# Kernel optimization log

Hardware: AMD Instinct MI355X
Metric: run time of the kernel (lower is better)

The kernel has to match this reference:

```python
import jax, jax.numpy as jnp
import numpy as np

B, D_IN, D_BN, K = 4096, 4096, 32768, 64

def setup_inputs() -> dict:
    key = jax.random.key(0)
    k1, k2, k3 = jax.random.split(key, 3)
    x = jax.random.normal(k1, (B, D_IN), dtype=jnp.float32)
    # encoder weight [bottleneck, input], kaiming-ish scale
    W_enc = jax.random.normal(k2, (D_BN, D_IN), dtype=jnp.float32) / np.sqrt(D_IN)
    b_enc = jax.random.normal(k3, (D_BN,), dtype=jnp.float32) * 0.01
    b_dec = jnp.zeros((D_IN,), dtype=jnp.float32)
    return {"x": x, "W_enc": W_enc, "b_enc": b_enc, "b_dec": b_dec, "k": K}

def reference(x, W_enc, b_enc, b_dec, k):
    # encode: z1 = x @ W_enc.T + b_enc  -> [B, bottleneck]
    a1 = jnp.einsum('bi,ni->bn', x, W_enc) + b_enc
    # top-k winner-take-all mask along latent dim (eval path: current_k = k)
    k_count = min(max(1, int(k)), a1.shape[1])
    _, topk_idx = jax.lax.top_k(a1, k_count)              # [B, k]
    rows = jnp.arange(a1.shape[0])[:, None]
    mask = jnp.zeros_like(a1).at[rows, topk_idx].set(1.0)
    a1 = a1 * mask
    # tied-weight decode: z2 = a1 @ W_enc + b_dec  -> [B, input]
    z2 = jnp.einsum('bn,ni->bi', a1, W_enc) + b_dec
    return z2
```

## Files before the change

kernel.cpp:

```cpp
#include <hip/hip_runtime.h>

#define M_DIM 4096
#define K_DIM 4096
#define N_DIM 32768
#define TOPK  64
#define NCAND 96
#define NT    (K_DIM / 64)

typedef __attribute__((ext_vector_type(8))) _Float16 half8;
typedef __attribute__((ext_vector_type(4))) _Float16 half4;
typedef __attribute__((ext_vector_type(4))) float    f32x4;

#define GLDS(gp, lp) __builtin_amdgcn_global_load_lds( \
    (const __attribute__((address_space(1))) void*)(gp), \
    (__attribute__((address_space(3))) void*)(lp), 16, 0, 0)

#define BARX()  asm volatile("s_barrier" ::: "memory")
#define LGKM0() asm volatile("s_waitcnt lgkmcnt(0)" ::: "memory")
#define VMC6()  asm volatile("s_waitcnt vmcnt(6)" ::: "memory")
#define VMC0()  asm volatile("s_waitcnt vmcnt(0)" ::: "memory")

__launch_bounds__(256)
__global__ void cast_kernel(const float4* __restrict__ src, half4* __restrict__ dst, int n4) {
  int i = blockIdx.x * blockDim.x + threadIdx.x;
  int stride = gridDim.x * blockDim.x;
  for (; i < n4; i += stride) {
    float4 x = src[i];
    half4 h;
    h[0] = (_Float16)x.x; h[1] = (_Float16)x.y; h[2] = (_Float16)x.z; h[3] = (_Float16)x.w;
    dst[i] = h;
  }
}

__launch_bounds__(512, 2)
__global__ void gemm_enc(const _Float16* __restrict__ xh, const _Float16* __restrict__ wh,
                         const float* __restrict__ b_enc, float* __restrict__ a1)
{
  __shared__ alignas(16) _Float16 lds[2 * 4 * 8192];

  const int tid  = threadIdx.x;
  const int lane = tid & 63;
  const int wave = tid >> 6;
  const int wm = wave >> 2;
  const int wn = wave & 3;

  const int bid  = blockIdx.x;
  const int xcd  = bid & 7;
  const int bi   = bid >> 3;
  const int ncol = xcd * 16 + (bi >> 4);
  const int mrow = bi & 15;
  const int m0 = mrow << 8;
  const int n0 = ncol << 8;

  const int srow   = tid >> 3;
  const int schunk = (tid & 7) ^ (srow & 7);
  const _Float16* pA = xh + (size_t)(m0 + srow) * K_DIM + schunk * 8;
  const _Float16* pB = wh + (size_t)(n0 + srow) * K_DIM + schunk * 8;
  const int sdst = tid * 8;

  const int l15 = lane & 15, l7 = lane & 7, kq = lane >> 4;
  const int c0  = kq ^ l7;
  const int ck0 = c0 * 8, ck1 = (c0 ^ 4) * 8;
  const int arow = l15 * 64;
  const int brow = (wn & 1) * 4096 + l15 * 64;

  f32x4 acc[8][4];
  const f32x4 zero = {0.f, 0.f, 0.f, 0.f};
#pragma unroll
  for (int im = 0; im < 8; ++im)
#pragma unroll
    for (int jn = 0; jn < 4; ++jn) acc[im][jn] = zero;

#define STAGE(c, t) do { \
    const _Float16* sp_ = (((c) >= 2) ? pA : pB) + (size_t)((c) & 1) * 128 * K_DIM + (t) * 64; \
    _Float16* dp_ = &lds[(((((t) & 1) << 2) | (c)) << 13) + sdst]; \
    GLDS(sp_, dp_); \
    GLDS(sp_ + 64 * K_DIM, dp_ + 4096); \
  } while (0)

  half8 a_[4][2], b_[4][2];

#define LDA(mh, ab) do { \
    _Pragma("unroll") for (int mt = 0; mt < 4; ++mt) { \
      a_[mt][0] = *(const half8*)&lds[(ab) + (mh) * 4096 + mt * 1024 + arow + ck0]; \
      a_[mt][1] = *(const half8*)&lds[(ab) + (mh) * 4096 + mt * 1024 + arow + ck1]; \
    } } while (0)

#define LDB(bb) do { \
    _Pragma("unroll") for (int nt = 0; nt < 4; ++nt) { \
      b_[nt][0] = *(const half8*)&lds[(bb) + nt * 1024 + brow + ck0]; \
      b_[nt][1] = *(const half8*)&lds[(bb) + nt * 1024 + brow + ck1]; \
    } } while (0)

#define QUAD(mh, nh) do { \
    _Pragma("unroll") for (int mt = 0; mt < 4; ++mt) \
    _Pragma("unroll") for (int nt = 0; nt < 2; ++nt) { \
      acc[(mh)*4+mt][(nh)*2+nt] = __builtin_amdgcn_mfma_f32_16x16x32_f16( \
          a_[mt][0], b_[(nh)*2+nt][0], acc[(mh)*4+mt][(nh)*2+nt], 0, 0, 0); \
      acc[(mh)*4+mt][(nh)*2+nt] = __builtin_amdgcn_mfma_f32_16x16x32_f16( \
          a_[mt][1], b_[(nh)*2+nt][1], acc[(mh)*4+mt][(nh)*2+nt], 0, 0, 0); \
    } } while (0)

  STAGE(0, 0); STAGE(1, 0); STAGE(2, 0); STAGE(3, 0);
  STAGE(0, 1); STAGE(1, 1); STAGE(2, 1);
  VMC6();
  BARX();

  for (int T = 0; T < NT; ++T) {
    const int ab = (((T & 1) << 2) + 2 + wm) << 13;
    const int bb = (((T & 1) << 2) + (wn >> 1)) << 13;
    LDA(0, ab);
    LDB(bb);
    if (T + 1 < NT) STAGE(3, T + 1);
    BARX(); LGKM0();
    __builtin_amdgcn_s_setprio(1); QUAD(0, 0); __builtin_amdgcn_s_setprio(0);
    BARX();
    if (T + 2 < NT) STAGE(0, T + 2);
    BARX();
    __builtin_amdgcn_s_setprio(1); QUAD(0, 1); __builtin_amdgcn_s_setprio(0);
    BARX();
    LDA(1, ab);
    if (T + 2 < NT) STAGE(1, T + 2);
    BARX(); LGKM0();
    __builtin_amdgcn_s_setprio(1); QUAD(1, 0); __builtin_amdgcn_s_setprio(0);
    BARX();
    if (T + 2 < NT) STAGE(2, T + 2);
    BARX();
    __builtin_amdgcn_s_setprio(1); QUAD(1, 1); __builtin_amdgcn_s_setprio(0);
    if (T < NT - 2) { VMC6(); } else { VMC0(); }
    BARX();
  }

  const int col = lane & 15;
  const int r4  = (lane >> 4) << 2;
#pragma unroll
  for (int nt = 0; nt < 4; ++nt) {
    const int gc = n0 + wn * 64 + nt * 16 + col;
    const float bias = b_enc[gc];
#pragma unroll
    for (int mt = 0; mt < 8; ++mt) {
#pragma unroll
      for (int r = 0; r < 4; ++r) {
        const int gr = m0 + wm * 128 + mt * 16 + r4 + r;
        a1[(size_t)gr * N_DIM + gc] = acc[mt][nt][r] + bias;
      }
    }
  }
#undef STAGE
#undef LDA
#undef LDB
#undef QUAD
}

#define TK_THREADS 512
#define TK_PER 64
__launch_bounds__(512)
__global__ void topk_kernel(const float* __restrict__ a1, int* __restrict__ cand)
{
  const int row = blockIdx.x;
  const float* pr = a1 + (size_t)row * N_DIM;
  const int tid = threadIdx.x;

  unsigned u[TK_PER];
#pragma unroll
  for (int i = 0; i < TK_PER; ++i) {
    union { float f; unsigned b; } c;
    c.f = pr[i * TK_THREADS + tid];
    u[i] = (c.b & 0x80000000u) ? ~c.b : (c.b | 0x80000000u);
  }

  __shared__ int red[8];
  unsigned prefix = 0;
  int needed = NCAND;
  for (int bit = 31; bit >= 0; --bit) {
    unsigned want = (prefix >> bit) | 1u;
    int cnt = 0;
#pragma unroll
    for (int i = 0; i < TK_PER; ++i) cnt += ((u[i] >> bit) == want) ? 1 : 0;
    for (int off = 32; off > 0; off >>= 1) cnt += __shfl_down(cnt, off);
    if ((tid & 63) == 0) red[tid >> 6] = cnt;
    __syncthreads();
    int total = red[0] + red[1] + red[2] + red[3] + red[4] + red[5] + red[6] + red[7];
    __syncthreads();
    if (total >= needed) prefix |= (1u << bit);
    else needed -= total;
  }
  __shared__ int c_gt, c_tie;
  if (tid == 0) { c_gt = 0; c_tie = 0; }
  __syncthreads();
#pragma unroll
  for (int i = 0; i < TK_PER; ++i) {
    if (u[i] > prefix) {
      int p = atomicAdd(&c_gt, 1);
      cand[row * NCAND + p] = i * TK_THREADS + tid;
    }
  }
  __syncthreads();
  int base = c_gt;
#pragma unroll
  for (int i = 0; i < TK_PER; ++i) {
    if (u[i] == prefix) {
      int t = atomicAdd(&c_tie, 1);
      if (t < needed) cand[row * NCAND + base + t] = i * TK_THREADS + tid;
    }
  }
}

__launch_bounds__(256)
__global__ void refine_kernel(const float* __restrict__ x, const float* __restrict__ W,
                              const float* __restrict__ b_enc, const int* __restrict__ cand,
                              int* __restrict__ tk_idx, float* __restrict__ tk_val)
{
  const int row = blockIdx.x;
  const int tid = threadIdx.x, lane = tid & 63, wave = tid >> 6;
  __shared__ float svals[NCAND];
  __shared__ int   sidx[NCAND];
  __shared__ int   spos;

  const float* xr = x + (size_t)row * K_DIM;
  float4 xv[16];
#pragma unroll
  for (int c = 0; c < 16; ++c) xv[c] = *(const float4*)(xr + c * 256 + lane * 4);

  for (int j = wave; j < NCAND; j += 4) {
    int cj = cand[row * NCAND + j];
    const float* wr = W + (size_t)cj * K_DIM;
    float acc = 0.f;
#pragma unroll
    for (int c = 0; c < 16; ++c) {
      float4 wv = *(const float4*)(wr + c * 256 + lane * 4);
      acc += xv[c].x * wv.x + xv[c].y * wv.y + xv[c].z * wv.z + xv[c].w * wv.w;
    }
#pragma unroll
    for (int off = 32; off > 0; off >>= 1) acc += __shfl_down(acc, off, 64);
    if (lane == 0) { svals[j] = acc + b_enc[cj]; sidx[j] = cj; }
  }
  if (tid == 0) spos = 0;
  __syncthreads();

  if (tid < NCAND) {
    float v = svals[tid];
    int myidx = sidx[tid];
    int rank = 0;
    for (int i = 0; i < NCAND; ++i) {
      float vi = svals[i];
      rank += (vi > v || (vi == v && sidx[i] < myidx)) ? 1 : 0;
    }
    if (rank < TOPK) {
      int p = atomicAdd(&spos, 1);
      tk_idx[row * TOPK + p] = myidx;
      tk_val[row * TOPK + p] = v;
    }
  }
}

__launch_bounds__(256)
__global__ void decode_kernel(const _Float16* __restrict__ wh, const int* __restrict__ tk_idx,
                              const float* __restrict__ tk_val, const float* __restrict__ b_dec,
                              float* __restrict__ out)
{
  const int row = blockIdx.x, tid = threadIdx.x;
  __shared__ int   sidx[TOPK];
  __shared__ float sval[TOPK];
  if (tid < TOPK) { sidx[tid] = tk_idx[row * TOPK + tid]; sval[tid] = tk_val[row * TOPK + tid]; }
  __syncthreads();

  const int c0 = tid * 8;
  const int c1 = (tid + 256) * 8;
  float acc0[8], acc1[8];
#pragma unroll
  for (int e = 0; e < 8; ++e) { acc0[e] = b_dec[c0 + e]; acc1[e] = b_dec[c1 + e]; }

  for (int j = 0; j < TOPK; ++j) {
    const _Float16* wr = wh + (size_t)sidx[j] * K_DIM;
    half8 w0 = *(const half8*)(wr + c0);
    half8 w1 = *(const half8*)(wr + c1);
    float v = sval[j];
#pragma unroll
    for (int e = 0; e < 8; ++e) { acc0[e] += v * (float)w0[e]; acc1[e] += v * (float)w1[e]; }
  }
  float* po = out + (size_t)row * K_DIM;
#pragma unroll
  for (int e = 0; e < 8; ++e) { po[c0 + e] = acc0[e]; po[c1 + e] = acc1[e]; }
}

extern "C" void kernel_launch(void* const* d_in, const int* in_sizes, int n_in,
                              void* d_out, int out_size, void* d_ws, size_t ws_size,
                              hipStream_t stream) {
  const float* x     = (const float*)d_in[0];
  const float* W     = (const float*)d_in[1];
  const float* b_enc = (const float*)d_in[2];
  const float* b_dec = (const float*)d_in[3];

  _Float16* x_h = (_Float16*)d_ws;
  _Float16* w_h = x_h + (size_t)M_DIM * K_DIM;
  float*    a1  = (float*)(w_h + (size_t)N_DIM * K_DIM);
  int*      cand = (int*)(a1 + (size_t)M_DIM * N_DIM);
  int*      tk_idx = cand + (size_t)M_DIM * NCAND;
  float*    tk_val = (float*)(tk_idx + M_DIM * TOPK);

  cast_kernel<<<4096, 256, 0, stream>>>((const float4*)x, (half4*)x_h,
                                        (int)((size_t)M_DIM * K_DIM / 4));
  cast_kernel<<<8192, 256, 0, stream>>>((const float4*)W, (half4*)w_h,
                                        (int)((size_t)N_DIM * K_DIM / 4));
  gemm_enc<<<(M_DIM / 256) * (N_DIM / 256), 512, 0, stream>>>(x_h, w_h, b_enc, a1);
  topk_kernel<<<M_DIM, TK_THREADS, 0, stream>>>(a1, cand);
  refine_kernel<<<M_DIM, 256, 0, stream>>>(x, W, b_enc, cand, tk_idx, tk_val);
  decode_kernel<<<M_DIM, 256, 0, stream>>>(w_h, tk_idx, tk_val, b_dec, (float*)d_out);
}
```

Baseline: 3.729 ms.

## Invert candidate refinement to group by latent column, staging each W row in LDS

Refinement is now split into four kernels. One clears per-latent counters, one scatters each row's candidate entries into per-latent buckets, one recomputes the exact fp32 dot products per latent, and one selects the top-k per row. The per-latent kernel loads each touched W row once into LDS and gathers x rows instead. That replaces thousands of random 16KB W-row reads with reads from the much smaller x matrix. It adds launches and atomics, and any latent with more than NCAND candidate rows silently drops entries, which would leave their values uninitialized.

```diff
diff --git a/kernel.cpp b/kernel.cpp
--- a/kernel.cpp
+++ b/kernel.cpp
@@ -207,35 +207,67 @@
 }
 
 __launch_bounds__(256)
-__global__ void refine_kernel(const float* __restrict__ x, const float* __restrict__ W,
-                              const float* __restrict__ b_enc, const int* __restrict__ cand,
+__global__ void clear_kernel(int* __restrict__ counts) {
+  int i = blockIdx.x * 256 + threadIdx.x;
+  if (i < N_DIM) counts[i] = 0;
+}
+
+__launch_bounds__(256)
+__global__ void scatter_kernel(const int* __restrict__ cand, int* __restrict__ counts,
+                               int* __restrict__ entries) {
+  int i = blockIdx.x * 256 + threadIdx.x;
+  int cj = cand[i];
+  int row = i / NCAND;
+  int j = i - row * NCAND;
+  int pos = atomicAdd(&counts[cj], 1);
+  if (pos < NCAND) entries[cj * NCAND + pos] = (row << 7) | j;
+}
+
+__launch_bounds__(256)
+__global__ void rvals_kernel(const float* __restrict__ x, const float* __restrict__ W,
+                             const float* __restrict__ b_enc,
+                             const int* __restrict__ counts, const int* __restrict__ entries,
+                             float* __restrict__ vals)
+{
+  const int n = blockIdx.x;
+  int c = counts[n];
+  if (c == 0) return;
+  if (c > NCAND) c = NCAND;
+  __shared__ float sw[K_DIM];
+  const int tid = threadIdx.x, lane = tid & 63, wave = tid >> 6;
+  const float* wr = W + (size_t)n * K_DIM;
+#pragma unroll
+  for (int t = 0; t < 4; ++t)
+    *(float4*)&sw[t * 1024 + tid * 4] = *(const float4*)&wr[t * 1024 + tid * 4];
+  __syncthreads();
+  const float bias = b_enc[n];
+  for (int e = wave; e < c; e += 4) {
+    const int pk  = entries[n * NCAND + e];
+    const int row = pk >> 7, j = pk & 127;
+    const float* xr = x + (size_t)row * K_DIM;
+    float acc = 0.f;
+#pragma unroll
+    for (int cc = 0; cc < 16; ++cc) {
+      float4 xv = *(const float4*)&xr[cc * 256 + lane * 4];
+      float4 wv = *(const float4*)&sw[cc * 256 + lane * 4];
+      acc += xv.x * wv.x + xv.y * wv.y + xv.z * wv.z + xv.w * wv.w;
+    }
+#pragma unroll
+    for (int off = 32; off > 0; off >>= 1) acc += __shfl_down(acc, off, 64);
+    if (lane == 0) vals[row * NCAND + j] = acc + bias;
+  }
+}
+
+__launch_bounds__(128)
+__global__ void select_kernel(const int* __restrict__ cand, const float* __restrict__ vals,
                               int* __restrict__ tk_idx, float* __restrict__ tk_val)
 {
-  const int row = blockIdx.x;
-  const int tid = threadIdx.x, lane = tid & 63, wave = tid >> 6;
+  const int row = blockIdx.x, tid = threadIdx.x;
   __shared__ float svals[NCAND];
   __shared__ int   sidx[NCAND];
   __shared__ int   spos;
-
-  const float* xr = x + (size_t)row * K_DIM;
-  float4 xv[16];
-#pragma unroll
-  for (int c = 0; c < 16; ++c) xv[c] = *(const float4*)(xr + c * 256 + lane * 4);
-
-  for (int j = wave; j < NCAND; j += 4) {
-    int cj = cand[row * NCAND + j];
-    const float* wr = W + (size_t)cj * K_DIM;
-    float acc = 0.f;
-#pragma unroll
-    for (int c = 0; c < 16; ++c) {
-      float4 wv = *(const float4*)(wr + c * 256 + lane * 4);
-      acc += xv[c].x * wv.x + xv[c].y * wv.y + xv[c].z * wv.z + xv[c].w * wv.w;
-    }
-#pragma unroll
-    for (int off = 32; off > 0; off >>= 1) acc += __shfl_down(acc, off, 64);
-    if (lane == 0) { svals[j] = acc + b_enc[cj]; sidx[j] = cj; }
-  }
   if (tid == 0) spos = 0;
+  if (tid < NCAND) { svals[tid] = vals[row * NCAND + tid]; sidx[tid] = cand[row * NCAND + tid]; }
   __syncthreads();
 
   if (tid < NCAND) {
@@ -299,12 +331,19 @@
   int*      tk_idx = cand + (size_t)M_DIM * NCAND;
   float*    tk_val = (float*)(tk_idx + M_DIM * TOPK);
 
+  int*   counts  = (int*)a1;
+  int*   entries = counts + N_DIM;
+  float* vals    = (float*)(entries + (size_t)N_DIM * NCAND);
+
   cast_kernel<<<4096, 256, 0, stream>>>((const float4*)x, (half4*)x_h,
                                         (int)((size_t)M_DIM * K_DIM / 4));
   cast_kernel<<<8192, 256, 0, stream>>>((const float4*)W, (half4*)w_h,
                                         (int)((size_t)N_DIM * K_DIM / 4));
   gemm_enc<<<(M_DIM / 256) * (N_DIM / 256), 512, 0, stream>>>(x_h, w_h, b_enc, a1);
   topk_kernel<<<M_DIM, TK_THREADS, 0, stream>>>(a1, cand);
-  refine_kernel<<<M_DIM, 256, 0, stream>>>(x, W, b_enc, cand, tk_idx, tk_val);
+  clear_kernel<<<N_DIM / 256, 256, 0, stream>>>(counts);
+  scatter_kernel<<<(M_DIM * NCAND) / 256, 256, 0, stream>>>(cand, counts, entries);
+  rvals_kernel<<<N_DIM, 256, 0, stream>>>(x, W, b_enc, counts, entries, vals);
+  select_kernel<<<M_DIM, 128, 0, stream>>>(cand, vals, tk_idx, tk_val);
   decode_kernel<<<M_DIM, 256, 0, stream>>>(w_h, tk_idx, tk_val, b_dec, (float*)d_out);
 }
```

Result: no change. 3.732 ms (+0.1%).

## Recompute only ambiguous top-k candidates in fp32, accept clear winners directly

Applied to the files above, without the earlier changes.

Adds a mark kernel that compares the fp16-GEMM activations of the 96 candidates within a fixed margin. Candidates clearly inside the top 64 are written straight to the output list using their fp16-derived values. Only the ambiguous ones around the cutoff are recomputed with fp32 dot products and ranked for the remaining slots. This is meant to cut the gathered fp32 reads of W rows and the dot-product work in the refine step. The trade-off is that accepted values keep fp16-accumulated precision, and correctness depends on the margin bounding the fp16 error.

```diff
diff --git a/kernel.cpp b/kernel.cpp
--- a/kernel.cpp
+++ b/kernel.cpp
@@ -19,6 +19,8 @@
 #define LGKM0() asm volatile("s_waitcnt lgkmcnt(0)" ::: "memory")
 #define VMC6()  asm volatile("s_waitcnt vmcnt(6)" ::: "memory")
 #define VMC0()  asm volatile("s_waitcnt vmcnt(0)" ::: "memory")
+
+#define MARGIN2 0.04f
 
 __launch_bounds__(256)
 __global__ void cast_kernel(const float4* __restrict__ src, half4* __restrict__ dst, int n4) {
@@ -206,24 +208,68 @@
   }
 }
 
+__launch_bounds__(128)
+__global__ void mark_kernel(const float* __restrict__ a1, const int* __restrict__ cand,
+                            int* __restrict__ nIn, int* __restrict__ nAmb,
+                            int* __restrict__ ambIdx,
+                            int* __restrict__ tk_idx, float* __restrict__ tk_val)
+{
+  const int row = blockIdx.x, tid = threadIdx.x;
+  __shared__ float sv[NCAND];
+  __shared__ int   si[NCAND];
+  __shared__ int cin, camb;
+  if (tid == 0) { cin = 0; camb = 0; }
+  if (tid < NCAND) {
+    int cj = cand[row * NCAND + tid];
+    si[tid] = cj;
+    sv[tid] = a1[(size_t)row * N_DIM + cj];
+  }
+  __syncthreads();
+  if (tid < NCAND) {
+    float v = sv[tid];
+    int above = 0, below = 0;
+    for (int j = 0; j < NCAND; ++j) {
+      above += (sv[j] > v + MARGIN2) ? 1 : 0;
+      below += (sv[j] < v - MARGIN2) ? 1 : 0;
+    }
+    if (below >= NCAND - TOPK) {
+      int p = atomicAdd(&cin, 1);
+      tk_idx[row * TOPK + p] = si[tid];
+      tk_val[row * TOPK + p] = v;
+    } else if (above < TOPK) {
+      int q = atomicAdd(&camb, 1);
+      ambIdx[row * NCAND + q] = si[tid];
+    }
+  }
+  __syncthreads();
+  if (tid == 0) { nIn[row] = cin; nAmb[row] = camb; }
+}
+
 __launch_bounds__(256)
-__global__ void refine_kernel(const float* __restrict__ x, const float* __restrict__ W,
-                              const float* __restrict__ b_enc, const int* __restrict__ cand,
+__global__ void refine_select(const float* __restrict__ x, const float* __restrict__ W,
+                              const float* __restrict__ b_enc,
+                              const int* __restrict__ nIn, const int* __restrict__ nAmb,
+                              const int* __restrict__ ambIdx,
                               int* __restrict__ tk_idx, float* __restrict__ tk_val)
 {
   const int row = blockIdx.x;
+  const int na = nAmb[row];
+  if (na == 0) return;
+  const int ni = nIn[row];
+  const int need = TOPK - ni;
   const int tid = threadIdx.x, lane = tid & 63, wave = tid >> 6;
-  __shared__ float svals[NCAND];
-  __shared__ int   sidx[NCAND];
-  __shared__ int   spos;
+  __shared__ float ev[NCAND];
+  __shared__ int   ei[NCAND];
+  __shared__ int spos;
+  if (tid == 0) spos = 0;
 
   const float* xr = x + (size_t)row * K_DIM;
   float4 xv[16];
 #pragma unroll
   for (int c = 0; c < 16; ++c) xv[c] = *(const float4*)(xr + c * 256 + lane * 4);
 
-  for (int j = wave; j < NCAND; j += 4) {
-    int cj = cand[row * NCAND + j];
+  for (int e = wave; e < na; e += 4) {
+    int cj = ambIdx[row * NCAND + e];
     const float* wr = W + (size_t)cj * K_DIM;
     float acc = 0.f;
 #pragma unroll
@@ -233,23 +279,22 @@
     }
 #pragma unroll
     for (int off = 32; off > 0; off >>= 1) acc += __shfl_down(acc, off, 64);
-    if (lane == 0) { svals[j] = acc + b_enc[cj]; sidx[j] = cj; }
-  }
-  if (tid == 0) spos = 0;
-  __syncthreads();
-
-  if (tid < NCAND) {
-    float v = svals[tid];
-    int myidx = sidx[tid];
+    if (lane == 0) { ev[e] = acc + b_enc[cj]; ei[e] = cj; }
+  }
+  __syncthreads();
+
+  if (tid < na && need > 0) {
+    float v = ev[tid];
+    int my = ei[tid];
     int rank = 0;
-    for (int i = 0; i < NCAND; ++i) {
-      float vi = svals[i];
-      rank += (vi > v || (vi == v && sidx[i] < myidx)) ? 1 : 0;
-    }
-    if (rank < TOPK) {
+    for (int i = 0; i < na; ++i) {
+      float vi = ev[i];
+      rank += (vi > v || (vi == v && ei[i] < my)) ? 1 : 0;
+    }
+    if (rank < need) {
       int p = atomicAdd(&spos, 1);
-      tk_idx[row * TOPK + p] = myidx;
-      tk_val[row * TOPK + p] = v;
+      tk_idx[row * TOPK + ni + p] = my;
+      tk_val[row * TOPK + ni + p] = v;
     }
   }
 }
@@ -299,12 +344,17 @@
   int*      tk_idx = cand + (size_t)M_DIM * NCAND;
   float*    tk_val = (float*)(tk_idx + M_DIM * TOPK);
 
+  int* nIn    = (int*)x_h;
+  int* nAmb   = nIn + M_DIM;
+  int* ambIdx = nAmb + M_DIM;
+
   cast_kernel<<<4096, 256, 0, stream>>>((const float4*)x, (half4*)x_h,
                                         (int)((size_t)M_DIM * K_DIM / 4));
   cast_kernel<<<8192, 256, 0, stream>>>((const float4*)W, (half4*)w_h,
                                         (int)((size_t)N_DIM * K_DIM / 4));
   gemm_enc<<<(M_DIM / 256) * (N_DIM / 256), 512, 0, stream>>>(x_h, w_h, b_enc, a1);
   topk_kernel<<<M_DIM, TK_THREADS, 0, stream>>>(a1, cand);
-  refine_kernel<<<M_DIM, 256, 0, stream>>>(x, W, b_enc, cand, tk_idx, tk_val);
+  mark_kernel<<<M_DIM, 128, 0, stream>>>(a1, cand, nIn, nAmb, ambIdx, tk_idx, tk_val);
+  refine_select<<<M_DIM, 256, 0, stream>>>(x, W, b_enc, nIn, nAmb, ambIdx, tk_idx, tk_val);
   decode_kernel<<<M_DIM, 256, 0, stream>>>(w_h, tk_idx, tk_val, b_dec, (float*)d_out);
 }
```

Result: faster. 2.997 ms (-19.6%).
